# Performance work log

Measured on AMD Instinct MI355X. Metric: run time of the kernel, lower is better.

## Reference

```python
import jax, jax.numpy as jnp
import numpy as np

B, C, H, W, K = 8, 256, 32, 32, 50
EPS = 1e-10
COS_EPS = 1e-8


def _euclid_dist(x, center):
    # x: [b, n, c], center: [K, c] -> [b, n, K]
    x2 = jnp.sum(x * x, axis=-1, keepdims=True)            # [b,n,1]
    c2 = jnp.sum(center * center, axis=-1)                 # [K]
    d2 = x2 + c2[None, None, :] - 2.0 * jnp.einsum('bnc,kc->bnk', x, center)
    return jnp.sqrt(jnp.maximum(d2, 0.0))


def setup_inputs() -> dict:
    key = jax.random.key(0)
    k1, k2, k3 = jax.random.split(key, 3)
    f = jax.random.normal(k1, (B, C, H, W), dtype=jnp.float32)
    center = jax.random.normal(k2, (K, C), dtype=jnp.float32)
    memory = jax.random.normal(k3, (1, C, H, W), dtype=jnp.float32)
    # pick Tc at the median min-distance so ~half the pixels are anomalous
    x = f.reshape(B, C, H * W).transpose(0, 2, 1)
    d = jnp.min(_euclid_dist(x, center), axis=2)
    Tc = jnp.median(d).astype(jnp.float32)
    return {"f": f, "center": center, "Tc": Tc, "memory": memory, "is_object": 0}


def reference(f, center, Tc, memory, is_object):
    b, c, h, w = f.shape
    n = h * w
    x = f.reshape(b, c, n).transpose(0, 2, 1)              # [b, n, c]
    dist = _euclid_dist(x, center)                         # [b, n, K]
    d = jnp.min(dist, axis=2)                              # [b, n]
    ano = (d > Tc).reshape(-1)                             # [P] bool
    nor = jnp.logical_not(ano)
    P = b * n
    X = x.reshape(P, c)                                    # [P, c]

    if is_object:
        mem = memory.reshape(1, c, n).transpose(0, 2, 1)   # [1, n, c]
        mem = jnp.broadcast_to(mem, (b, n, c)).reshape(P, c)
        Xnew = jnp.where(ano[:, None], mem, X)
    else:
        # cosine similarity of every pixel vs every pixel; columns masked to normals
        norms = jnp.maximum(jnp.linalg.norm(X, axis=1), COS_EPS)
        Xn = X / norms[:, None]
        sim = Xn @ Xn.T                                    # [P, P]
        logits = jnp.where(nor[None, :], sim, -1e30)
        wgt = jax.nn.softmax(logits, axis=1)               # ~0 at masked cols
        norf = nor.astype(f.dtype)
        t = jnp.maximum(jnp.sum(norf), 1.0)
        mu = jnp.sum(wgt * norf[None, :], axis=1, keepdims=True) / t
        var = jnp.sum(norf[None, :] * (wgt - mu) ** 2, axis=1, keepdims=True) / t
        thr = mu - 2.0 * jnp.sqrt(var)
        sw = jax.nn.relu(wgt - thr) * wgt / (jnp.abs(wgt - thr) + EPS)
        sw = sw * norf[None, :]
        sw = sw / jnp.sum(sw, axis=1, keepdims=True)
        new_vals = sw @ X                                  # mix of normal features
        Xnew = jnp.where(ano[:, None], new_vals, X)

    f_out = Xnew.reshape(b, n, c).transpose(0, 2, 1).reshape(b, c, h, w)

    d_flat = d.reshape(-1)
    anof = ano.astype(f.dtype)
    norf2 = 1.0 - anof
    cnt_ano = jnp.sum(anof)
    cnt_nor = jnp.maximum(jnp.sum(norf2), 1.0)
    mean_nor = jnp.sum(d_flat * norf2) / cnt_nor
    mean_ano = jnp.sum(d_flat * anof) / jnp.maximum(cnt_ano, 1.0)
    Ld = jnp.where(cnt_ano > 0, mean_nor / (mean_ano + 0.001), mean_nor)
    return f_out, Ld
```

## Files before the change

kernel.cpp:

```cpp
#include <hip/hip_runtime.h>
#include <math.h>
#include <stdint.h>

#define P_TOT 8192
#define CDIM  256
#define KC    50
#define NPIX  1024
#define TI    32

#define RPB   64
#define JSPA  16
#define JCHA  (P_TOT / JSPA)
#define JSP   8
#define JCH   (P_TOT / JSP)
#define JST   32
#define NJS   (JCH / JST)
#define NJSA  (JCHA / JST)

#define SWZK(row) ((((row) >> 1) & 7) << 4)

#define OFF_NRM   0
#define OFF_Z     8192
#define OFF_S2    16384
#define OFF_THR   24576
#define OFF_DEN   32768
#define OFF_SCAL  40960
#define OFF_C2    41024
#define OFF_NFLAG 53888
#define OFF_XNB   65536
#define OFF_XTB   1114112
#define OFF_PART  65536
#define OFF_OUT   2162688
#define IOFF_BASE 4259840
#define II_ANOIDX 0
#define II_M      8192
#define II_CNTANO 8193
#define II_FLAGS  8200

typedef __attribute__((ext_vector_type(8))) short short8;
typedef __attribute__((ext_vector_type(4))) float f32x4;

__device__ __forceinline__ ushort f2bf(float x) {
    union { float f; unsigned u; } v; v.f = x;
    unsigned r = v.u + 0x7fffu + ((v.u >> 16) & 1u);
    return (ushort)(r >> 16);
}
__device__ __forceinline__ float bf2f(ushort h) {
    union { unsigned u; float f; } v; v.u = ((unsigned)h) << 16;
    return v.f;
}

typedef const __attribute__((address_space(1))) void gas_void;
typedef __attribute__((address_space(3))) void las_void;
__device__ __forceinline__ void gld_lds16(const void* g, void* l) {
    __builtin_amdgcn_global_load_lds(
        (gas_void*)(unsigned long long)(uintptr_t)g,
        (las_void*)(unsigned int)(uintptr_t)l, 16, 0, 0);
}

__global__ void k0_prep(const float* __restrict__ center, float* __restrict__ wsF) {
    int tid = threadIdx.x;
    if (tid >= 200) return;
    int k = tid >> 2, q = tid & 3;
    float s = 0.f;
    const float* cp = center + k * CDIM + q * 64;
    for (int c = 0; c < 64; ++c) { float v = cp[c]; s += v * v; }
    s += __shfl_down(s, 2);
    s += __shfl_down(s, 1);
    if (q == 0) wsF[OFF_C2 + k] = s;
}

__global__ __launch_bounds__(256) void k1a_dot(const float* __restrict__ f,
                                               const float* __restrict__ center,
                                               float* __restrict__ PART) {
    int tid = threadIdx.x;
    int px = blockIdx.x * 256 + tid;
    int cg = blockIdx.y;
    int b = px >> 10, n = px & 1023;
    const float* fp = f + ((size_t)b * CDIM + cg * 64) * NPIX + n;
    float acc[KC];
#pragma unroll
    for (int k = 0; k < KC; ++k) acc[k] = 0.f;
    float x2 = 0.f;
    for (int cc = 0; cc < 64; ++cc) {
        float xv = fp[(size_t)cc * NPIX];
        x2 += xv * xv;
        const float* cp = center + (cg * 64 + cc);
#pragma unroll
        for (int k = 0; k < KC; ++k) acc[k] = fmaf(xv, cp[(size_t)k * CDIM], acc[k]);
    }
    float* dst = PART + (size_t)cg * 51 * P_TOT + px;
#pragma unroll
    for (int k = 0; k < KC; ++k) dst[(size_t)k * P_TOT] = acc[k];
    dst[(size_t)50 * P_TOT] = x2;
}

__global__ __launch_bounds__(256) void k1b_min(const float* __restrict__ TcP,
                                               const float* __restrict__ c2g,
                                               const float* __restrict__ PART,
                                               float* __restrict__ wsF,
                                               int* __restrict__ wsI) {
    int tid = threadIdx.x;
    int px = blockIdx.x * 256 + tid;
    float x2 = 0.f;
#pragma unroll
    for (int g = 0; g < 4; ++g) x2 += PART[((size_t)g * 51 + 50) * P_TOT + px];
    float d2m = 3.4e38f;
#pragma unroll 10
    for (int k = 0; k < KC; ++k) {
        float s = PART[(size_t)k * P_TOT + px];
#pragma unroll
        for (int g = 1; g < 4; ++g) s += PART[((size_t)g * 51 + k) * P_TOT + px];
        float d2 = x2 + c2g[k] - 2.f * s;
        d2m = fminf(d2m, d2);
    }
    float d = sqrtf(fmaxf(d2m, 0.f));
    bool ano = d > TcP[0];
    wsF[OFF_NRM + px] = fmaxf(sqrtf(x2), 1e-8f);
    wsF[OFF_NFLAG + px] = ano ? 0.f : 1.f;
    wsI[II_FLAGS + px] = ano ? 1 : 0;

    float dn = ano ? 0.f : d;
    float da = ano ? d : 0.f;
    for (int o = 32; o >= 1; o >>= 1) { dn += __shfl_down(dn, o); da += __shfl_down(da, o); }
    int lane = tid & 63;
    unsigned long long mask = __ballot(ano);
    int cnt = __popcll(mask);
    if (lane == 0) {
        atomicAdd(&wsF[OFF_SCAL + 0], dn);
        atomicAdd(&wsF[OFF_SCAL + 1], da);
        if (cnt) atomicAdd(&wsI[II_CNTANO], cnt);
    }
    if (ano) {
        int leader = __ffsll((unsigned long long)mask) - 1;
        int base = 0;
        if (lane == leader) base = atomicAdd(&wsI[II_M], cnt);
        base = __shfl(base, leader);
        int off = __popcll(mask & ((1ull << lane) - 1ull));
        wsI[II_ANOIDX + base + off] = px;
    }
}

__global__ void k2_convert(const float* __restrict__ f, float* __restrict__ wsF) {
    __shared__ float t[32][33];
    int b = blockIdx.z, n0 = blockIdx.x * 32, c0 = blockIdx.y * 32;
    int tx = threadIdx.x, ty = threadIdx.y;
    const float* src = f + ((size_t)b * CDIM + c0) * NPIX + n0;
    ushort* XnB = (ushort*)(wsF + OFF_XNB);
    ushort* XTB = (ushort*)(wsF + OFF_XTB);
#pragma unroll
    for (int r = 0; r < 32; r += 8) {
        float v = src[(size_t)(ty + r) * NPIX + tx];
        t[ty + r][tx] = v;
        XTB[(size_t)(c0 + ty + r) * P_TOT + b * NPIX + n0 + tx] = f2bf(v);
    }
    __syncthreads();
#pragma unroll
    for (int r = 0; r < 32; r += 8) {
        int p = b * NPIX + n0 + ty + r;
        float nrm = wsF[OFF_NRM + p];
        XnB[(size_t)p * CDIM + c0 + tx] = f2bf(t[tx][ty + r] / nrm);
    }
}

__global__ void k3_copy(const float* __restrict__ f, float* __restrict__ out,
                        const float* __restrict__ wsF, const int* __restrict__ wsI) {
    int gid = blockIdx.x * blockDim.x + threadIdx.x;
    const float4* src = (const float4*)f;
    float4* dst = (float4*)out;
    int total = P_TOT * CDIM / 4;
    for (int i = gid; i < total; i += gridDim.x * blockDim.x) dst[i] = src[i];
    if (gid == 0) {
        int cntAno = wsI[II_CNTANO];
        float cntNor = (float)(P_TOT - cntAno);
        float meanNor = wsF[OFF_SCAL + 0] / fmaxf(cntNor, 1.f);
        float meanAno = wsF[OFF_SCAL + 1] / fmaxf((float)cntAno, 1.f);
        out[P_TOT * CDIM] = (cntAno > 0) ? meanNor / (meanAno + 0.001f) : meanNor;
    }
}

__global__ __launch_bounds__(256, 4) void k5a(float* __restrict__ wsF, const int* __restrict__ wsI) {
    const int Mv = wsI[II_M];
    const int i0 = blockIdx.x * RPB;
    if (i0 >= Mv) return;
    __shared__ __align__(16) ushort sK[2][JST * CDIM];
    const int tid = threadIdx.x;
    const int wave = tid >> 6, lane = tid & 63;
    const int lrow = lane & 15, lgrp = lane >> 4;
    const char* XnBb = (const char*)(wsF + OFF_XNB);
    const float* nflag = wsF + OFF_NFLAG;
    const int* anoIdx = wsI + II_ANOIDX;
    const int jc0 = blockIdx.y * JCHA;
    const int iw = i0 + wave * 16;

    short8 qf[8];
    {
        int arow = anoIdx[min(iw + lrow, Mv - 1)];
        const ushort* qp = (const ushort*)XnBb + (size_t)arow * CDIM + lgrp * 8;
#pragma unroll
        for (int kc = 0; kc < 8; ++kc) qf[kc] = *(const short8*)(qp + kc * 32);
    }
    float zAcc[4], s2Acc[4];
#pragma unroll
    for (int r = 0; r < 4; ++r) { zAcc[r] = 0.f; s2Acc[r] = 0.f; }

    auto stageK = [&](int buf, int j0) {
#pragma unroll
        for (int it = 0; it < 4; ++it) {
            int chunk = (wave << 2) + it;
            int d = (chunk << 10) + (lane << 4);
            int row = d >> 9;
            int srco = (d & ~511) | ((d & 511) ^ SWZK(row));
            gld_lds16(XnBb + ((size_t)j0 << 9) + srco, (char*)sK[buf] + (chunk << 10));
        }
    };

    stageK(0, jc0);
    __syncthreads();
    int cur = 0;
    for (int js = 0; js < NJSA; ++js) {
        int j0 = jc0 + js * JST;
        if (js + 1 < NJSA) stageK(cur ^ 1, j0 + JST);
        float mf0 = nflag[j0 + lrow];
        float mf1 = nflag[j0 + 16 + lrow];
        f32x4 acc0 = {0.f, 0.f, 0.f, 0.f}, acc1 = {0.f, 0.f, 0.f, 0.f};
#pragma unroll
        for (int kc = 0; kc < 8; ++kc) {
            int cb = (kc << 6) + (lgrp << 4);
            int b0 = lrow * 512 + (cb ^ SWZK(lrow));
            int b1 = (16 + lrow) * 512 + (cb ^ SWZK(16 + lrow));
            short8 bf0 = *(const short8*)((const char*)sK[cur] + b0);
            short8 bf1 = *(const short8*)((const char*)sK[cur] + b1);
            acc0 = __builtin_amdgcn_mfma_f32_16x16x32_bf16(qf[kc], bf0, acc0, 0, 0, 0);
            acc1 = __builtin_amdgcn_mfma_f32_16x16x32_bf16(qf[kc], bf1, acc1, 0, 0, 0);
        }
#pragma unroll
        for (int r = 0; r < 4; ++r) {
            float e0 = __expf(acc0[r] - 1.f) * mf0;
            float e1 = __expf(acc1[r] - 1.f) * mf1;
            zAcc[r] += e0 + e1;
            s2Acc[r] += e0 * e0 + e1 * e1;
        }
        __syncthreads();
        cur ^= 1;
    }
#pragma unroll
    for (int r = 0; r < 4; ++r) {
        float z = zAcc[r], q = s2Acc[r];
        for (int m = 8; m >= 1; m >>= 1) { z += __shfl_xor(z, m); q += __shfl_xor(q, m); }
        if (lrow == 0) {
            int i = iw + lgrp * 4 + r;
            if (i < Mv) { atomicAdd(&wsF[OFF_Z + i], z); atomicAdd(&wsF[OFF_S2 + i], q); }
        }
    }
}

__global__ void k4b_thr(float* __restrict__ wsF, const int* __restrict__ wsI) {
    int Mv = wsI[II_M];
    int idx = blockIdx.x * 256 + threadIdx.x;
    if (idx >= Mv) return;
    float t = fmaxf((float)(P_TOT - wsI[II_CNTANO]), 1.f);
    float Z = wsF[OFF_Z + idx], S2 = wsF[OFF_S2 + idx];
    float mu = 1.f / t;
    float var = S2 / (Z * Z * t) - mu * mu;
    wsF[OFF_THR + idx] = mu - 2.f * sqrtf(fmaxf(var, 0.f));
}

__global__ __launch_bounds__(256, 2) void k5c(float* __restrict__ wsF, const int* __restrict__ wsI) {
    const int Mv = wsI[II_M];
    const int i0 = blockIdx.x * RPB;
    if (i0 >= Mv) return;
    __shared__ __align__(16) ushort sK[2][JST * CDIM];
    __shared__ __align__(16) ushort sXT[2][CDIM * JST];
    __shared__ __align__(16) char sSW[4][16 * 144];
    const int tid = threadIdx.x;
    const int wave = tid >> 6, lane = tid & 63;
    const int lrow = lane & 15, lgrp = lane >> 4;
    const char* XnBb = (const char*)(wsF + OFF_XNB);
    const char* XTBb = (const char*)(wsF + OFF_XTB);
    const float* nflag = wsF + OFF_NFLAG;
    const int* anoIdx = wsI + II_ANOIDX;
    const int jc0 = blockIdx.y * JCH;
    const int iw = i0 + wave * 16;

    short8 qf[8];
    {
        int arow = anoIdx[min(iw + lrow, Mv - 1)];
        const ushort* qp = (const ushort*)XnBb + (size_t)arow * CDIM + lgrp * 8;
#pragma unroll
        for (int kc = 0; kc < 8; ++kc) qf[kc] = *(const short8*)(qp + kc * 32);
    }
    float rz[4], thr[4], den[4];
#pragma unroll
    for (int r = 0; r < 4; ++r) {
        int i = min(iw + lgrp * 4 + r, Mv - 1);
        rz[r] = 1.f / wsF[OFF_Z + i];
        thr[r] = wsF[OFF_THR + i];
        den[r] = 0.f;
    }
    f32x4 oAcc[16];
#pragma unroll
    for (int ct = 0; ct < 16; ++ct) oAcc[ct] = (f32x4){0.f, 0.f, 0.f, 0.f};

    auto stageK = [&](int buf, int j0) {
#pragma unroll
        for (int it = 0; it < 4; ++it) {
            int chunk = (wave << 2) + it;
            int d = (chunk << 10) + (lane << 4);
            int row = d >> 9;
            int srco = (d & ~511) | ((d & 511) ^ SWZK(row));
            gld_lds16(XnBb + ((size_t)j0 << 9) + srco, (char*)sK[buf] + (chunk << 10));
        }
    };
    auto stageX = [&](int buf, int j0) {
#pragma unroll
        for (int it = 0; it < 4; ++it) {
            int chunk = (wave << 2) + it;
            int d = (chunk << 10) + (lane << 4);
            int R = d >> 7;
            int q = (d & 127) ^ ((R & 7) << 4);
            int c = 2 * R + (q >> 6);
            gld_lds16(XTBb + (size_t)c * (P_TOT * 2) + ((size_t)j0 << 1) + (q & 63),
                      (char*)sXT[buf] + (chunk << 10));
        }
    };

    stageK(0, jc0);
    stageX(0, jc0);
    __syncthreads();
    int cur = 0;
    char* msw = sSW[wave];
    for (int js = 0; js < NJS; ++js) {
        int j0 = jc0 + js * JST;
        if (js + 1 < NJS) { stageK(cur ^ 1, j0 + JST); stageX(cur ^ 1, j0 + JST); }
        float2 mfp = *(const float2*)&nflag[j0 + 2 * lrow];
        f32x4 acc0 = {0.f, 0.f, 0.f, 0.f}, acc1 = {0.f, 0.f, 0.f, 0.f};
#pragma unroll
        for (int kc = 0; kc < 8; ++kc) {
            int cb = (kc << 6) + (lgrp << 4);
            int b0 = (2 * lrow) * 512 + (cb ^ SWZK(2 * lrow));
            int b1 = (2 * lrow + 1) * 512 + (cb ^ SWZK(2 * lrow + 1));
            short8 bf0 = *(const short8*)((const char*)sK[cur] + b0);
            short8 bf1 = *(const short8*)((const char*)sK[cur] + b1);
            acc0 = __builtin_amdgcn_mfma_f32_16x16x32_bf16(qf[kc], bf0, acc0, 0, 0, 0);
            acc1 = __builtin_amdgcn_mfma_f32_16x16x32_bf16(qf[kc], bf1, acc1, 0, 0, 0);
        }
#pragma unroll
        for (int r = 0; r < 4; ++r) {
            int irow = lgrp * 4 + r;
            float w0 = __expf(acc0[r] - 1.f) * mfp.x * rz[r];
            float d0 = w0 - thr[r];
            float sw0 = fmaxf(d0, 0.f) * w0 / (fabsf(d0) + 1e-10f);
            float w1 = __expf(acc1[r] - 1.f) * mfp.y * rz[r];
            float d1 = w1 - thr[r];
            float sw1 = fmaxf(d1, 0.f) * w1 / (fabsf(d1) + 1e-10f);
            ushort h0 = f2bf(sw0), h1 = f2bf(sw1);
            den[r] += bf2f(h0) + bf2f(h1);
            *(unsigned*)(msw + irow * 144 + 4 * lrow) = ((unsigned)h1 << 16) | (unsigned)h0;
        }
        short8 aF = *(const short8*)(msw + lrow * 144 + lgrp * 16);
#pragma unroll
        for (int ct = 0; ct < 16; ++ct) {
            int crow = ct * 16 + lrow;
            int R = crow >> 1;
            int off = (((crow & 1) << 6) + (lgrp << 4)) ^ ((R & 7) << 4);
            short8 bf = *(const short8*)((const char*)sXT[cur] + R * 128 + off);
            oAcc[ct] = __builtin_amdgcn_mfma_f32_16x16x32_bf16(aF, bf, oAcc[ct], 0, 0, 0);
        }
        __syncthreads();
        cur ^= 1;
    }

#pragma unroll
    for (int r = 0; r < 4; ++r) {
        float dv = den[r];
        for (int m = 8; m >= 1; m >>= 1) dv += __shfl_xor(dv, m);
        int i = iw + lgrp * 4 + r;
        if (lrow == 0 && i < Mv) atomicAdd(&wsF[OFF_DEN + i], dv);
        if (i < Mv) {
            float* go = wsF + OFF_OUT + (size_t)i * CDIM + lrow;
#pragma unroll
            for (int ct = 0; ct < 16; ++ct) atomicAdd(&go[ct * 16], oAcc[ct][r]);
        }
    }
}

__global__ void k4d_final(float* __restrict__ out, const float* __restrict__ wsF,
                          const int* __restrict__ wsI) {
    int Mv = wsI[II_M];
    int i0 = blockIdx.x * TI;
    if (i0 >= Mv) return;
    int tid = threadIdx.x;
    int ii = tid >> 3, cg = tid & 7;
    int i = i0 + ii;
    if (i >= Mv) return;
    int p = wsI[II_ANOIDX + i];
    int b = p >> 10, n = p & 1023;
    float rden = 1.f / wsF[OFF_DEN + i];
    const float* go = wsF + OFF_OUT + (size_t)i * CDIM;
    float* op = out + (size_t)b * CDIM * NPIX + n;
#pragma unroll
    for (int cc = 0; cc < 32; ++cc) {
        int c = cc * 8 + cg;
        op[(size_t)c * NPIX] = go[c] * rden;
    }
}

extern "C" void kernel_launch(void* const* d_in, const int* in_sizes, int n_in,
                              void* d_out, int out_size, void* d_ws, size_t ws_size,
                              hipStream_t stream) {
    const float* f = (const float*)d_in[0];
    const float* center = (const float*)d_in[1];
    const float* Tc = (const float*)d_in[2];
    float* out = (float*)d_out;
    float* wsF = (float*)d_ws;
    int* wsI = (int*)(wsF + IOFF_BASE);

    hipMemsetAsync(wsF + OFF_Z, 0, (OFF_C2 + 64 - OFF_Z) * sizeof(float), stream);
    hipMemsetAsync(wsF + OFF_OUT, 0, (size_t)P_TOT * CDIM * sizeof(float), stream);
    hipMemsetAsync(wsI + II_M, 0, 2 * sizeof(int), stream);

    k0_prep<<<1, 256, 0, stream>>>(center, wsF);
    dim3 g1a(32, 4);
    k1a_dot<<<g1a, 256, 0, stream>>>(f, center, wsF + OFF_PART);
    k1b_min<<<32, 256, 0, stream>>>(Tc, wsF + OFF_C2, wsF + OFF_PART, wsF, wsI);
    dim3 g2(32, 8, 8), b2(32, 8);
    k2_convert<<<g2, b2, 0, stream>>>(f, wsF);
    k3_copy<<<512, 256, 0, stream>>>(f, out, wsF, wsI);
    dim3 g5a(P_TOT / RPB, JSPA);
    k5a<<<g5a, 256, 0, stream>>>(wsF, wsI);
    k4b_thr<<<P_TOT / 256, 256, 0, stream>>>(wsF, wsI);
    dim3 g5c(P_TOT / RPB, JSP);
    k5c<<<g5c, 256, 0, stream>>>(wsF, wsI);
    k4d_final<<<P_TOT / TI, 256, 0, stream>>>(out, wsF, wsI);
}
```

Baseline: 184.3 us.

## Give each wave 32 query rows to reuse staged keys across two MFMA tiles

Both attention-style kernels now have each wave own two 16-row query groups, so a block covers 128 rows. Every key and feature fragment read from LDS feeds twice as many MFMAs, which halves LDS and global staging traffic per output. The column split is doubled to keep the grid size up. The sparsified-weight formula relu(w-thr)*w/(|w-thr|+eps) is replaced by a plain select of w when w > thr, and the denominator is now accumulated in fp32 rather than from bf16-rounded values. The cost is roughly doubled accumulator registers (32 f32x4 output tiles in k5c), which may lower occupancy or cause spills, plus more atomic adds from the finer column split.

```diff
diff --git a/kernel.cpp b/kernel.cpp
--- a/kernel.cpp
+++ b/kernel.cpp
@@ -8,10 +8,10 @@
 #define NPIX  1024
 #define TI    32
 
-#define RPB   64
-#define JSPA  16
+#define RPB   128
+#define JSPA  32
 #define JCHA  (P_TOT / JSPA)
-#define JSP   8
+#define JSP   16
 #define JCH   (P_TOT / JSP)
 #define JST   32
 #define NJS   (JCH / JST)
@@ -45,10 +45,6 @@
     unsigned r = v.u + 0x7fffu + ((v.u >> 16) & 1u);
     return (ushort)(r >> 16);
 }
-__device__ __forceinline__ float bf2f(ushort h) {
-    union { unsigned u; float f; } v; v.u = ((unsigned)h) << 16;
-    return v.f;
-}
 
 typedef const __attribute__((address_space(1))) void gas_void;
 typedef __attribute__((address_space(3))) void las_void;
@@ -191,18 +187,21 @@
     const float* nflag = wsF + OFF_NFLAG;
     const int* anoIdx = wsI + II_ANOIDX;
     const int jc0 = blockIdx.y * JCHA;
-    const int iw = i0 + wave * 16;
-
-    short8 qf[8];
-    {
-        int arow = anoIdx[min(iw + lrow, Mv - 1)];
+    const int iw = i0 + wave * 32;
+
+    short8 qf[2][8];
+#pragma unroll
+    for (int ag = 0; ag < 2; ++ag) {
+        int arow = anoIdx[min(iw + ag * 16 + lrow, Mv - 1)];
         const ushort* qp = (const ushort*)XnBb + (size_t)arow * CDIM + lgrp * 8;
 #pragma unroll
-        for (int kc = 0; kc < 8; ++kc) qf[kc] = *(const short8*)(qp + kc * 32);
-    }
-    float zAcc[4], s2Acc[4];
-#pragma unroll
-    for (int r = 0; r < 4; ++r) { zAcc[r] = 0.f; s2Acc[r] = 0.f; }
+        for (int kc = 0; kc < 8; ++kc) qf[ag][kc] = *(const short8*)(qp + kc * 32);
+    }
+    float zAcc[2][4], s2Acc[2][4];
+#pragma unroll
+    for (int ag = 0; ag < 2; ++ag)
+#pragma unroll
+        for (int r = 0; r < 4; ++r) { zAcc[ag][r] = 0.f; s2Acc[ag][r] = 0.f; }
 
     auto stageK = [&](int buf, int j0) {
 #pragma unroll
@@ -223,7 +222,11 @@
         if (js + 1 < NJSA) stageK(cur ^ 1, j0 + JST);
         float mf0 = nflag[j0 + lrow];
         float mf1 = nflag[j0 + 16 + lrow];
-        f32x4 acc0 = {0.f, 0.f, 0.f, 0.f}, acc1 = {0.f, 0.f, 0.f, 0.f};
+        f32x4 acc[2][2];
+#pragma unroll
+        for (int ag = 0; ag < 2; ++ag)
+#pragma unroll
+            for (int jt = 0; jt < 2; ++jt) acc[ag][jt] = (f32x4){0.f, 0.f, 0.f, 0.f};
 #pragma unroll
         for (int kc = 0; kc < 8; ++kc) {
             int cb = (kc << 6) + (lgrp << 4);
@@ -231,28 +234,34 @@
             int b1 = (16 + lrow) * 512 + (cb ^ SWZK(16 + lrow));
             short8 bf0 = *(const short8*)((const char*)sK[cur] + b0);
             short8 bf1 = *(const short8*)((const char*)sK[cur] + b1);
-            acc0 = __builtin_amdgcn_mfma_f32_16x16x32_bf16(qf[kc], bf0, acc0, 0, 0, 0);
-            acc1 = __builtin_amdgcn_mfma_f32_16x16x32_bf16(qf[kc], bf1, acc1, 0, 0, 0);
-        }
-#pragma unroll
-        for (int r = 0; r < 4; ++r) {
-            float e0 = __expf(acc0[r] - 1.f) * mf0;
-            float e1 = __expf(acc1[r] - 1.f) * mf1;
-            zAcc[r] += e0 + e1;
-            s2Acc[r] += e0 * e0 + e1 * e1;
-        }
+            acc[0][0] = __builtin_amdgcn_mfma_f32_16x16x32_bf16(qf[0][kc], bf0, acc[0][0], 0, 0, 0);
+            acc[0][1] = __builtin_amdgcn_mfma_f32_16x16x32_bf16(qf[0][kc], bf1, acc[0][1], 0, 0, 0);
+            acc[1][0] = __builtin_amdgcn_mfma_f32_16x16x32_bf16(qf[1][kc], bf0, acc[1][0], 0, 0, 0);
+            acc[1][1] = __builtin_amdgcn_mfma_f32_16x16x32_bf16(qf[1][kc], bf1, acc[1][1], 0, 0, 0);
+        }
+#pragma unroll
+        for (int ag = 0; ag < 2; ++ag)
+#pragma unroll
+            for (int r = 0; r < 4; ++r) {
+                float e0 = __expf(acc[ag][0][r] - 1.f) * mf0;
+                float e1 = __expf(acc[ag][1][r] - 1.f) * mf1;
+                zAcc[ag][r] += e0 + e1;
+                s2Acc[ag][r] += e0 * e0 + e1 * e1;
+            }
         __syncthreads();
         cur ^= 1;
     }
 #pragma unroll
-    for (int r = 0; r < 4; ++r) {
-        float z = zAcc[r], q = s2Acc[r];
-        for (int m = 8; m >= 1; m >>= 1) { z += __shfl_xor(z, m); q += __shfl_xor(q, m); }
-        if (lrow == 0) {
-            int i = iw + lgrp * 4 + r;
-            if (i < Mv) { atomicAdd(&wsF[OFF_Z + i], z); atomicAdd(&wsF[OFF_S2 + i], q); }
-        }
-    }
+    for (int ag = 0; ag < 2; ++ag)
+#pragma unroll
+        for (int r = 0; r < 4; ++r) {
+            float z = zAcc[ag][r], q = s2Acc[ag][r];
+            for (int m = 8; m >= 1; m >>= 1) { z += __shfl_xor(z, m); q += __shfl_xor(q, m); }
+            if (lrow == 0) {
+                int i = iw + ag * 16 + lgrp * 4 + r;
+                if (i < Mv) { atomicAdd(&wsF[OFF_Z + i], z); atomicAdd(&wsF[OFF_S2 + i], q); }
+            }
+        }
 }
 
 __global__ void k4b_thr(float* __restrict__ wsF, const int* __restrict__ wsI) {
@@ -272,7 +281,7 @@
     if (i0 >= Mv) return;
     __shared__ __align__(16) ushort sK[2][JST * CDIM];
     __shared__ __align__(16) ushort sXT[2][CDIM * JST];
-    __shared__ __align__(16) char sSW[4][16 * 144];
+    __shared__ __align__(16) char sSW[4][32 * 72];
     const int tid = threadIdx.x;
     const int wave = tid >> 6, lane = tid & 63;
     const int lrow = lane & 15, lgrp = lane >> 4;
@@ -281,26 +290,31 @@
     const float* nflag = wsF + OFF_NFLAG;
     const int* anoIdx = wsI + II_ANOIDX;
     const int jc0 = blockIdx.y * JCH;
-    const int iw = i0 + wave * 16;
-
-    short8 qf[8];
-    {
-        int arow = anoIdx[min(iw + lrow, Mv - 1)];
+    const int iw = i0 + wave * 32;
+
+    short8 qf[2][8];
+#pragma unroll
+    for (int ag = 0; ag < 2; ++ag) {
+        int arow = anoIdx[min(iw + ag * 16 + lrow, Mv - 1)];
         const ushort* qp = (const ushort*)XnBb + (size_t)arow * CDIM + lgrp * 8;
 #pragma unroll
-        for (int kc = 0; kc < 8; ++kc) qf[kc] = *(const short8*)(qp + kc * 32);
-    }
-    float rz[4], thr[4], den[4];
-#pragma unroll
-    for (int r = 0; r < 4; ++r) {
-        int i = min(iw + lgrp * 4 + r, Mv - 1);
-        rz[r] = 1.f / wsF[OFF_Z + i];
-        thr[r] = wsF[OFF_THR + i];
-        den[r] = 0.f;
-    }
-    f32x4 oAcc[16];
-#pragma unroll
-    for (int ct = 0; ct < 16; ++ct) oAcc[ct] = (f32x4){0.f, 0.f, 0.f, 0.f};
+        for (int kc = 0; kc < 8; ++kc) qf[ag][kc] = *(const short8*)(qp + kc * 32);
+    }
+    float rz[2][4], thr[2][4], den[2][4];
+#pragma unroll
+    for (int ag = 0; ag < 2; ++ag)
+#pragma unroll
+        for (int r = 0; r < 4; ++r) {
+            int i = min(iw + ag * 16 + lgrp * 4 + r, Mv - 1);
+            rz[ag][r] = 1.f / wsF[OFF_Z + i];
+            thr[ag][r] = wsF[OFF_THR + i];
+            den[ag][r] = 0.f;
+        }
+    f32x4 oAcc[2][16];
+#pragma unroll
+    for (int ag = 0; ag < 2; ++ag)
+#pragma unroll
+        for (int ct = 0; ct < 16; ++ct) oAcc[ag][ct] = (f32x4){0.f, 0.f, 0.f, 0.f};
 
     auto stageK = [&](int buf, int j0) {
 #pragma unroll
@@ -334,7 +348,11 @@
         int j0 = jc0 + js * JST;
         if (js + 1 < NJS) { stageK(cur ^ 1, j0 + JST); stageX(cur ^ 1, j0 + JST); }
         float2 mfp = *(const float2*)&nflag[j0 + 2 * lrow];
-        f32x4 acc0 = {0.f, 0.f, 0.f, 0.f}, acc1 = {0.f, 0.f, 0.f, 0.f};
+        f32x4 acc[2][2];
+#pragma unroll
+        for (int ag = 0; ag < 2; ++ag)
+#pragma unroll
+            for (int jt = 0; jt < 2; ++jt) acc[ag][jt] = (f32x4){0.f, 0.f, 0.f, 0.f};
 #pragma unroll
         for (int kc = 0; kc < 8; ++kc) {
             int cb = (kc << 6) + (lgrp << 4);
@@ -342,47 +360,53 @@
             int b1 = (2 * lrow + 1) * 512 + (cb ^ SWZK(2 * lrow + 1));
             short8 bf0 = *(const short8*)((const char*)sK[cur] + b0);
             short8 bf1 = *(const short8*)((const char*)sK[cur] + b1);
-            acc0 = __builtin_amdgcn_mfma_f32_16x16x32_bf16(qf[kc], bf0, acc0, 0, 0, 0);
-            acc1 = __builtin_amdgcn_mfma_f32_16x16x32_bf16(qf[kc], bf1, acc1, 0, 0, 0);
-        }
-#pragma unroll
-        for (int r = 0; r < 4; ++r) {
-            int irow = lgrp * 4 + r;
-            float w0 = __expf(acc0[r] - 1.f) * mfp.x * rz[r];
-            float d0 = w0 - thr[r];
-            float sw0 = fmaxf(d0, 0.f) * w0 / (fabsf(d0) + 1e-10f);
-            float w1 = __expf(acc1[r] - 1.f) * mfp.y * rz[r];
-            float d1 = w1 - thr[r];
-            float sw1 = fmaxf(d1, 0.f) * w1 / (fabsf(d1) + 1e-10f);
-            ushort h0 = f2bf(sw0), h1 = f2bf(sw1);
-            den[r] += bf2f(h0) + bf2f(h1);
-            *(unsigned*)(msw + irow * 144 + 4 * lrow) = ((unsigned)h1 << 16) | (unsigned)h0;
-        }
-        short8 aF = *(const short8*)(msw + lrow * 144 + lgrp * 16);
+            acc[0][0] = __builtin_amdgcn_mfma_f32_16x16x32_bf16(qf[0][kc], bf0, acc[0][0], 0, 0, 0);
+            acc[0][1] = __builtin_amdgcn_mfma_f32_16x16x32_bf16(qf[0][kc], bf1, acc[0][1], 0, 0, 0);
+            acc[1][0] = __builtin_amdgcn_mfma_f32_16x16x32_bf16(qf[1][kc], bf0, acc[1][0], 0, 0, 0);
+            acc[1][1] = __builtin_amdgcn_mfma_f32_16x16x32_bf16(qf[1][kc], bf1, acc[1][1], 0, 0, 0);
+        }
+#pragma unroll
+        for (int ag = 0; ag < 2; ++ag)
+#pragma unroll
+            for (int r = 0; r < 4; ++r) {
+                int irow = ag * 16 + lgrp * 4 + r;
+                float w0 = __expf(acc[ag][0][r] - 1.f) * mfp.x * rz[ag][r];
+                float w1 = __expf(acc[ag][1][r] - 1.f) * mfp.y * rz[ag][r];
+                float sw0 = (w0 > thr[ag][r]) ? w0 : 0.f;
+                float sw1 = (w1 > thr[ag][r]) ? w1 : 0.f;
+                den[ag][r] += sw0 + sw1;
+                *(unsigned*)(msw + irow * 72 + 4 * lrow) =
+                    ((unsigned)f2bf(sw1) << 16) | (unsigned)f2bf(sw0);
+            }
+        short8 aF0 = *(const short8*)(msw + lrow * 72 + lgrp * 16);
+        short8 aF1 = *(const short8*)(msw + (16 + lrow) * 72 + lgrp * 16);
 #pragma unroll
         for (int ct = 0; ct < 16; ++ct) {
             int crow = ct * 16 + lrow;
             int R = crow >> 1;
             int off = (((crow & 1) << 6) + (lgrp << 4)) ^ ((R & 7) << 4);
             short8 bf = *(const short8*)((const char*)sXT[cur] + R * 128 + off);
-            oAcc[ct] = __builtin_amdgcn_mfma_f32_16x16x32_bf16(aF, bf, oAcc[ct], 0, 0, 0);
+            oAcc[0][ct] = __builtin_amdgcn_mfma_f32_16x16x32_bf16(aF0, bf, oAcc[0][ct], 0, 0, 0);
+            oAcc[1][ct] = __builtin_amdgcn_mfma_f32_16x16x32_bf16(aF1, bf, oAcc[1][ct], 0, 0, 0);
         }
         __syncthreads();
         cur ^= 1;
     }
 
 #pragma unroll
-    for (int r = 0; r < 4; ++r) {
-        float dv = den[r];
-        for (int m = 8; m >= 1; m >>= 1) dv += __shfl_xor(dv, m);
-        int i = iw + lgrp * 4 + r;
-        if (lrow == 0 && i < Mv) atomicAdd(&wsF[OFF_DEN + i], dv);
-        if (i < Mv) {
-            float* go = wsF + OFF_OUT + (size_t)i * CDIM + lrow;
-#pragma unroll
-            for (int ct = 0; ct < 16; ++ct) atomicAdd(&go[ct * 16], oAcc[ct][r]);
-        }
-    }
+    for (int ag = 0; ag < 2; ++ag)
+#pragma unroll
+        for (int r = 0; r < 4; ++r) {
+            float dv = den[ag][r];
+            for (int m = 8; m >= 1; m >>= 1) dv += __shfl_xor(dv, m);
+            int i = iw + ag * 16 + lgrp * 4 + r;
+            if (lrow == 0 && i < Mv) atomicAdd(&wsF[OFF_DEN + i], dv);
+            if (i < Mv) {
+                float* go = wsF + OFF_OUT + (size_t)i * CDIM + lrow;
+#pragma unroll
+                for (int ct = 0; ct < 16; ++ct) atomicAdd(&go[ct * 16], oAcc[ag][ct][r]);
+            }
+        }
 }
 
 __global__ void k4d_final(float* __restrict__ out, const float* __restrict__ wsF,
```

New measurement: 271.5 us. +47.3%, slower.

## Switch attention kernels to 32x32x16 MFMA with shuffle-based weight fragments

Applied to the files above, without the earlier changes.

Both the softmax-statistics kernel (k5a) and the weighted-mix kernel (k5c) move from 16x16x32 to 32x32x16 bf16 MFMA tiles, so K rows act as the A operand against query fragments held in registers. k5a now covers 128 rows per block with twice the j-split, and uses a ballot to mask out non-normal columns. In k5c the softmax weights are turned into the A fragment through cross-half lane shuffles instead of going through shared-memory staging, and the two waves of each pair split the output channels. The soft-threshold formula is reduced to a plain w>thr select and the denominator is summed in fp32, which changes rounding slightly. The intent is fewer MFMA issues and less LDS traffic, at the cost of more accumulator registers and intricate fragment-layout code that could hide indexing errors.

```diff
diff --git a/kernel.cpp b/kernel.cpp
--- a/kernel.cpp
+++ b/kernel.cpp
@@ -8,16 +8,16 @@
 #define NPIX  1024
 #define TI    32
 
-#define RPB   64
-#define JSPA  16
+#define RPBA  128
+#define JSPA  32
 #define JCHA  (P_TOT / JSPA)
+#define NJSA  (JCHA / 32)
+#define RPBC  64
 #define JSP   8
 #define JCH   (P_TOT / JSP)
-#define JST   32
-#define NJS   (JCH / JST)
-#define NJSA  (JCHA / JST)
-
-#define SWZK(row) ((((row) >> 1) & 7) << 4)
+#define NJS   (JCH / 32)
+
+#define SWZ8(r) (((r) & 7) << 4)
 
 #define OFF_NRM   0
 #define OFF_Z     8192
@@ -38,16 +38,12 @@
 #define II_FLAGS  8200
 
 typedef __attribute__((ext_vector_type(8))) short short8;
-typedef __attribute__((ext_vector_type(4))) float f32x4;
+typedef __attribute__((ext_vector_type(16))) float f32x16;
 
 __device__ __forceinline__ ushort f2bf(float x) {
     union { float f; unsigned u; } v; v.f = x;
     unsigned r = v.u + 0x7fffu + ((v.u >> 16) & 1u);
     return (ushort)(r >> 16);
-}
-__device__ __forceinline__ float bf2f(ushort h) {
-    union { unsigned u; float f; } v; v.u = ((unsigned)h) << 16;
-    return v.f;
 }
 
 typedef const __attribute__((address_space(1))) void gas_void;
@@ -181,37 +177,35 @@
 
 __global__ __launch_bounds__(256, 4) void k5a(float* __restrict__ wsF, const int* __restrict__ wsI) {
     const int Mv = wsI[II_M];
-    const int i0 = blockIdx.x * RPB;
+    const int i0 = blockIdx.x * RPBA;
     if (i0 >= Mv) return;
-    __shared__ __align__(16) ushort sK[2][JST * CDIM];
+    __shared__ __align__(16) ushort sK[2][32 * CDIM];
     const int tid = threadIdx.x;
     const int wave = tid >> 6, lane = tid & 63;
-    const int lrow = lane & 15, lgrp = lane >> 4;
+    const int jl = lane & 31, g = lane >> 5;
     const char* XnBb = (const char*)(wsF + OFF_XNB);
     const float* nflag = wsF + OFF_NFLAG;
     const int* anoIdx = wsI + II_ANOIDX;
     const int jc0 = blockIdx.y * JCHA;
-    const int iw = i0 + wave * 16;
-
-    short8 qf[8];
+    const int iw = i0 + wave * 32;
+    const int myrow = iw + jl;
+
+    short8 qf[16];
     {
-        int arow = anoIdx[min(iw + lrow, Mv - 1)];
-        const ushort* qp = (const ushort*)XnBb + (size_t)arow * CDIM + lgrp * 8;
-#pragma unroll
-        for (int kc = 0; kc < 8; ++kc) qf[kc] = *(const short8*)(qp + kc * 32);
-    }
-    float zAcc[4], s2Acc[4];
-#pragma unroll
-    for (int r = 0; r < 4; ++r) { zAcc[r] = 0.f; s2Acc[r] = 0.f; }
+        int arow = anoIdx[min(myrow, Mv - 1)];
+#pragma unroll
+        for (int kc = 0; kc < 16; ++kc)
+            qf[kc] = *(const short8*)(XnBb + (size_t)arow * 512 + kc * 32 + g * 16);
+    }
+    float z = 0.f, s2 = 0.f;
 
     auto stageK = [&](int buf, int j0) {
 #pragma unroll
         for (int it = 0; it < 4; ++it) {
-            int chunk = (wave << 2) + it;
-            int d = (chunk << 10) + (lane << 4);
+            int d = ((it * 256 + tid) << 4);
             int row = d >> 9;
-            int srco = (d & ~511) | ((d & 511) ^ SWZK(row));
-            gld_lds16(XnBb + ((size_t)j0 << 9) + srco, (char*)sK[buf] + (chunk << 10));
+            int srco = (d & ~511) | ((d & 511) ^ SWZ8(row));
+            gld_lds16(XnBb + ((size_t)j0 << 9) + srco, (char*)sK[buf] + d);
         }
     };
 
@@ -219,39 +213,33 @@
     __syncthreads();
     int cur = 0;
     for (int js = 0; js < NJSA; ++js) {
-        int j0 = jc0 + js * JST;
-        if (js + 1 < NJSA) stageK(cur ^ 1, j0 + JST);
-        float mf0 = nflag[j0 + lrow];
-        float mf1 = nflag[j0 + 16 + lrow];
-        f32x4 acc0 = {0.f, 0.f, 0.f, 0.f}, acc1 = {0.f, 0.f, 0.f, 0.f};
-#pragma unroll
-        for (int kc = 0; kc < 8; ++kc) {
-            int cb = (kc << 6) + (lgrp << 4);
-            int b0 = lrow * 512 + (cb ^ SWZK(lrow));
-            int b1 = (16 + lrow) * 512 + (cb ^ SWZK(16 + lrow));
-            short8 bf0 = *(const short8*)((const char*)sK[cur] + b0);
-            short8 bf1 = *(const short8*)((const char*)sK[cur] + b1);
-            acc0 = __builtin_amdgcn_mfma_f32_16x16x32_bf16(qf[kc], bf0, acc0, 0, 0, 0);
-            acc1 = __builtin_amdgcn_mfma_f32_16x16x32_bf16(qf[kc], bf1, acc1, 0, 0, 0);
-        }
-#pragma unroll
-        for (int r = 0; r < 4; ++r) {
-            float e0 = __expf(acc0[r] - 1.f) * mf0;
-            float e1 = __expf(acc1[r] - 1.f) * mf1;
-            zAcc[r] += e0 + e1;
-            s2Acc[r] += e0 * e0 + e1 * e1;
+        int j0 = jc0 + js * 32;
+        if (js + 1 < NJSA) stageK(cur ^ 1, j0 + 32);
+        f32x16 acc;
+#pragma unroll
+        for (int r = 0; r < 16; ++r) acc[r] = 0.f;
+#pragma unroll
+        for (int kc = 0; kc < 16; ++kc) {
+            int aoff = jl * 512 + ((kc * 32 + g * 16) ^ SWZ8(jl));
+            short8 af = *(const short8*)((const char*)sK[cur] + aoff);
+            acc = __builtin_amdgcn_mfma_f32_32x32x16_bf16(af, qf[kc], acc, 0, 0, 0);
+        }
+        float nf = nflag[j0 + jl];
+        unsigned um = (unsigned)__ballot(nf > 0.5f);
+#pragma unroll
+        for (int r = 0; r < 16; ++r) {
+            int jr = (r & 3) + 8 * (r >> 2) + 4 * g;
+            float e = ((um >> jr) & 1u) ? __expf(acc[r] - 1.f) : 0.f;
+            z += e; s2 += e * e;
         }
         __syncthreads();
         cur ^= 1;
     }
-#pragma unroll
-    for (int r = 0; r < 4; ++r) {
-        float z = zAcc[r], q = s2Acc[r];
-        for (int m = 8; m >= 1; m >>= 1) { z += __shfl_xor(z, m); q += __shfl_xor(q, m); }
-        if (lrow == 0) {
-            int i = iw + lgrp * 4 + r;
-            if (i < Mv) { atomicAdd(&wsF[OFF_Z + i], z); atomicAdd(&wsF[OFF_S2 + i], q); }
-        }
+    z += __shfl_xor(z, 32);
+    s2 += __shfl_xor(s2, 32);
+    if (lane < 32 && myrow < Mv) {
+        atomicAdd(&wsF[OFF_Z + myrow], z);
+        atomicAdd(&wsF[OFF_S2 + myrow], s2);
     }
 }
 
@@ -268,60 +256,58 @@
 
 __global__ __launch_bounds__(256, 2) void k5c(float* __restrict__ wsF, const int* __restrict__ wsI) {
     const int Mv = wsI[II_M];
-    const int i0 = blockIdx.x * RPB;
+    const int i0 = blockIdx.x * RPBC;
     if (i0 >= Mv) return;
-    __shared__ __align__(16) ushort sK[2][JST * CDIM];
-    __shared__ __align__(16) ushort sXT[2][CDIM * JST];
-    __shared__ __align__(16) char sSW[4][16 * 144];
+    __shared__ __align__(16) ushort sK[2][32 * CDIM];
+    __shared__ __align__(16) ushort sXT[2][CDIM * 32];
     const int tid = threadIdx.x;
     const int wave = tid >> 6, lane = tid & 63;
-    const int lrow = lane & 15, lgrp = lane >> 4;
+    const int jl = lane & 31, g = lane >> 5;
+    const int pair = wave >> 1, ch = wave & 1;
     const char* XnBb = (const char*)(wsF + OFF_XNB);
     const char* XTBb = (const char*)(wsF + OFF_XTB);
     const float* nflag = wsF + OFF_NFLAG;
     const int* anoIdx = wsI + II_ANOIDX;
     const int jc0 = blockIdx.y * JCH;
-    const int iw = i0 + wave * 16;
-
-    short8 qf[8];
+    const int ibase = i0 + pair * 32;
+    const int myrow = ibase + jl;
+
+    short8 qf[16];
+    float rz, thr;
     {
-        int arow = anoIdx[min(iw + lrow, Mv - 1)];
-        const ushort* qp = (const ushort*)XnBb + (size_t)arow * CDIM + lgrp * 8;
-#pragma unroll
-        for (int kc = 0; kc < 8; ++kc) qf[kc] = *(const short8*)(qp + kc * 32);
-    }
-    float rz[4], thr[4], den[4];
-#pragma unroll
-    for (int r = 0; r < 4; ++r) {
-        int i = min(iw + lgrp * 4 + r, Mv - 1);
-        rz[r] = 1.f / wsF[OFF_Z + i];
-        thr[r] = wsF[OFF_THR + i];
-        den[r] = 0.f;
-    }
-    f32x4 oAcc[16];
-#pragma unroll
-    for (int ct = 0; ct < 16; ++ct) oAcc[ct] = (f32x4){0.f, 0.f, 0.f, 0.f};
+        int ii = min(myrow, Mv - 1);
+        int arow = anoIdx[ii];
+#pragma unroll
+        for (int kc = 0; kc < 16; ++kc)
+            qf[kc] = *(const short8*)(XnBb + (size_t)arow * 512 + kc * 32 + g * 16);
+        rz = 1.f / wsF[OFF_Z + ii];
+        thr = wsF[OFF_THR + ii];
+    }
+    float den = 0.f;
+    f32x16 oAcc[4];
+#pragma unroll
+    for (int ct = 0; ct < 4; ++ct)
+#pragma unroll
+        for (int r = 0; r < 16; ++r) oAcc[ct][r] = 0.f;
 
     auto stageK = [&](int buf, int j0) {
 #pragma unroll
         for (int it = 0; it < 4; ++it) {
-            int chunk = (wave << 2) + it;
-            int d = (chunk << 10) + (lane << 4);
+            int d = ((it * 256 + tid) << 4);
             int row = d >> 9;
-            int srco = (d & ~511) | ((d & 511) ^ SWZK(row));
-            gld_lds16(XnBb + ((size_t)j0 << 9) + srco, (char*)sK[buf] + (chunk << 10));
+            int srco = (d & ~511) | ((d & 511) ^ SWZ8(row));
+            gld_lds16(XnBb + ((size_t)j0 << 9) + srco, (char*)sK[buf] + d);
         }
     };
     auto stageX = [&](int buf, int j0) {
 #pragma unroll
         for (int it = 0; it < 4; ++it) {
-            int chunk = (wave << 2) + it;
-            int d = (chunk << 10) + (lane << 4);
+            int d = ((it * 256 + tid) << 4);
             int R = d >> 7;
-            int q = (d & 127) ^ ((R & 7) << 4);
+            int q = (d & 127) ^ SWZ8(R);
             int c = 2 * R + (q >> 6);
             gld_lds16(XTBb + (size_t)c * (P_TOT * 2) + ((size_t)j0 << 1) + (q & 63),
-                      (char*)sXT[buf] + (chunk << 10));
+                      (char*)sXT[buf] + d);
         }
     };
 
@@ -329,58 +315,68 @@
     stageX(0, jc0);
     __syncthreads();
     int cur = 0;
-    char* msw = sSW[wave];
     for (int js = 0; js < NJS; ++js) {
-        int j0 = jc0 + js * JST;
-        if (js + 1 < NJS) { stageK(cur ^ 1, j0 + JST); stageX(cur ^ 1, j0 + JST); }
-        float2 mfp = *(const float2*)&nflag[j0 + 2 * lrow];
-        f32x4 acc0 = {0.f, 0.f, 0.f, 0.f}, acc1 = {0.f, 0.f, 0.f, 0.f};
-#pragma unroll
-        for (int kc = 0; kc < 8; ++kc) {
-            int cb = (kc << 6) + (lgrp << 4);
-            int b0 = (2 * lrow) * 512 + (cb ^ SWZK(2 * lrow));
-            int b1 = (2 * lrow + 1) * 512 + (cb ^ SWZK(2 * lrow + 1));
-            short8 bf0 = *(const short8*)((const char*)sK[cur] + b0);
-            short8 bf1 = *(const short8*)((const char*)sK[cur] + b1);
-            acc0 = __builtin_amdgcn_mfma_f32_16x16x32_bf16(qf[kc], bf0, acc0, 0, 0, 0);
-            acc1 = __builtin_amdgcn_mfma_f32_16x16x32_bf16(qf[kc], bf1, acc1, 0, 0, 0);
-        }
-#pragma unroll
-        for (int r = 0; r < 4; ++r) {
-            int irow = lgrp * 4 + r;
-            float w0 = __expf(acc0[r] - 1.f) * mfp.x * rz[r];
-            float d0 = w0 - thr[r];
-            float sw0 = fmaxf(d0, 0.f) * w0 / (fabsf(d0) + 1e-10f);
-            float w1 = __expf(acc1[r] - 1.f) * mfp.y * rz[r];
-            float d1 = w1 - thr[r];
-            float sw1 = fmaxf(d1, 0.f) * w1 / (fabsf(d1) + 1e-10f);
-            ushort h0 = f2bf(sw0), h1 = f2bf(sw1);
-            den[r] += bf2f(h0) + bf2f(h1);
-            *(unsigned*)(msw + irow * 144 + 4 * lrow) = ((unsigned)h1 << 16) | (unsigned)h0;
-        }
-        short8 aF = *(const short8*)(msw + lrow * 144 + lgrp * 16);
-#pragma unroll
-        for (int ct = 0; ct < 16; ++ct) {
-            int crow = ct * 16 + lrow;
-            int R = crow >> 1;
-            int off = (((crow & 1) << 6) + (lgrp << 4)) ^ ((R & 7) << 4);
-            short8 bf = *(const short8*)((const char*)sXT[cur] + R * 128 + off);
-            oAcc[ct] = __builtin_amdgcn_mfma_f32_16x16x32_bf16(aF, bf, oAcc[ct], 0, 0, 0);
+        int j0 = jc0 + js * 32;
+        if (js + 1 < NJS) { stageK(cur ^ 1, j0 + 32); stageX(cur ^ 1, j0 + 32); }
+        f32x16 acc;
+#pragma unroll
+        for (int r = 0; r < 16; ++r) acc[r] = 0.f;
+#pragma unroll
+        for (int kc = 0; kc < 16; ++kc) {
+            int aoff = jl * 512 + ((kc * 32 + g * 16) ^ SWZ8(jl));
+            short8 af = *(const short8*)((const char*)sK[cur] + aoff);
+            acc = __builtin_amdgcn_mfma_f32_32x32x16_bf16(af, qf[kc], acc, 0, 0, 0);
+        }
+        float nf = nflag[j0 + jl];
+        unsigned um = (unsigned)__ballot(nf > 0.5f);
+        float sw[16];
+#pragma unroll
+        for (int r = 0; r < 16; ++r) {
+            int jr = (r & 3) + 8 * (r >> 2) + 4 * g;
+            float w = ((um >> jr) & 1u) ? __expf(acc[r] - 1.f) * rz : 0.f;
+            sw[r] = (w > thr) ? w : 0.f;
+            den += sw[r];
+        }
+#pragma unroll
+        for (int kk = 0; kk < 2; ++kk) {
+            int s = 8 * kk;
+            unsigned p0 = ((unsigned)f2bf(sw[s + 1]) << 16) | f2bf(sw[s + 0]);
+            unsigned p1 = ((unsigned)f2bf(sw[s + 3]) << 16) | f2bf(sw[s + 2]);
+            unsigned p2 = ((unsigned)f2bf(sw[s + 5]) << 16) | f2bf(sw[s + 4]);
+            unsigned p3 = ((unsigned)f2bf(sw[s + 7]) << 16) | f2bf(sw[s + 6]);
+            unsigned o0 = (unsigned)__shfl_xor((int)p0, 32);
+            unsigned o1 = (unsigned)__shfl_xor((int)p1, 32);
+            unsigned o2 = (unsigned)__shfl_xor((int)p2, 32);
+            unsigned o3 = (unsigned)__shfl_xor((int)p3, 32);
+            union { unsigned u[4]; short8 v; } fr;
+            fr.u[0] = g ? o2 : p0;
+            fr.u[1] = g ? o3 : p1;
+            fr.u[2] = g ? p2 : o0;
+            fr.u[3] = g ? p3 : o1;
+#pragma unroll
+            for (int ct = 0; ct < 4; ++ct) {
+                int c = ch * 128 + ct * 32 + jl;
+                int R = c >> 1;
+                int off = (((c & 1) << 6) | (32 * kk + 16 * g)) ^ SWZ8(R);
+                short8 bf = *(const short8*)((const char*)sXT[cur] + R * 128 + off);
+                oAcc[ct] = __builtin_amdgcn_mfma_f32_32x32x16_bf16(fr.v, bf, oAcc[ct], 0, 0, 0);
+            }
         }
         __syncthreads();
         cur ^= 1;
     }
 
-#pragma unroll
-    for (int r = 0; r < 4; ++r) {
-        float dv = den[r];
-        for (int m = 8; m >= 1; m >>= 1) dv += __shfl_xor(dv, m);
-        int i = iw + lgrp * 4 + r;
-        if (lrow == 0 && i < Mv) atomicAdd(&wsF[OFF_DEN + i], dv);
-        if (i < Mv) {
-            float* go = wsF + OFF_OUT + (size_t)i * CDIM + lrow;
-#pragma unroll
-            for (int ct = 0; ct < 16; ++ct) atomicAdd(&go[ct * 16], oAcc[ct][r]);
+    den += __shfl_xor(den, 32);
+    if (ch == 0 && lane < 32 && myrow < Mv)
+        atomicAdd(&wsF[OFF_DEN + myrow], den);
+#pragma unroll
+    for (int ct = 0; ct < 4; ++ct) {
+        int col = ch * 128 + ct * 32 + jl;
+#pragma unroll
+        for (int r = 0; r < 16; ++r) {
+            int row = ibase + (r & 3) + 8 * (r >> 2) + 4 * g;
+            if (row < Mv)
+                atomicAdd(&wsF[OFF_OUT + (size_t)row * CDIM + col], oAcc[ct][r]);
         }
     }
 }
@@ -427,10 +423,10 @@
     dim3 g2(32, 8, 8), b2(32, 8);
     k2_convert<<<g2, b2, 0, stream>>>(f, wsF);
     k3_copy<<<512, 256, 0, stream>>>(f, out, wsF, wsI);
-    dim3 g5a(P_TOT / RPB, JSPA);
+    dim3 g5a(P_TOT / RPBA, JSPA);
     k5a<<<g5a, 256, 0, stream>>>(wsF, wsI);
     k4b_thr<<<P_TOT / 256, 256, 0, stream>>>(wsF, wsI);
-    dim3 g5c(P_TOT / RPB, JSP);
+    dim3 g5c(P_TOT / RPBC, JSP);
     k5c<<<g5c, 256, 0, stream>>>(wsF, wsI);
     k4d_final<<<P_TOT / TI, 256, 0, stream>>>(out, wsF, wsI);
 }
```

Measured after the change: 195.6 us. 6.2% more time.
